# Kernel tuning notes

Measured on AMD Instinct MI355X. Metric: run time of the kernel, lower is better.

## Reference

```python
import jax, jax.numpy as jnp
import numpy as np

N_NODES = 50000
N_EDGES = 800000
IN_FEATS = 64
H_FEATS = 128


def _uniform(key, shape, stdv):
    return jax.random.uniform(key, shape, jnp.float32, -stdv, stdv)


def setup_inputs() -> dict:
    key = jax.random.key(0)
    ks = jax.random.split(key, 16)
    inp = {}
    inp["features"] = jax.random.normal(ks[0], (N_NODES, IN_FEATS), jnp.float32)
    inp["mask"] = (jax.random.uniform(ks[1], (N_NODES, IN_FEATS)) > 0.3).astype(jnp.float32)
    inp["norm_g"] = jax.random.uniform(ks[2], (N_NODES, 1), jnp.float32, 0.05, 1.0)
    inp["norm_f"] = jax.random.uniform(ks[3], (N_NODES, 1), jnp.float32, 0.05, 1.0)
    inp["src_g"] = jax.random.randint(ks[4], (N_EDGES,), 0, N_NODES, jnp.int32)
    inp["dst_g"] = jax.random.randint(ks[5], (N_EDGES,), 0, N_NODES, jnp.int32)
    inp["src_f"] = jax.random.randint(ks[6], (N_EDGES,), 0, N_NODES, jnp.int32)
    inp["dst_f"] = jax.random.randint(ks[7], (N_EDGES,), 0, N_NODES, jnp.int32)
    # learned params, init per reset_parameters (uniform +/- 1/sqrt(out_feats))
    s1 = 1.0 / np.sqrt(H_FEATS)
    inp["W1"] = _uniform(ks[8], (IN_FEATS, H_FEATS), s1)
    inp["b1"] = _uniform(ks[9], (H_FEATS,), s1)
    s2 = 1.0 / np.sqrt(IN_FEATS)
    inp["wh"] = _uniform(ks[10], (H_FEATS, IN_FEATS), s2)
    inp["bh"] = _uniform(ks[11], (IN_FEATS,), s2)
    inp["ws"] = _uniform(ks[12], (IN_FEATS, IN_FEATS), s2)
    inp["bs"] = _uniform(ks[13], (IN_FEATS,), s2)
    return inp


def _aggregate(h, src, dst):
    # DGL update_all(copy_src, sum): gather source node feats per edge, sum at dst
    return jax.ops.segment_sum(h[src], dst, num_segments=N_NODES)


def reference(features, mask, norm_g, norm_f, src_g, dst_g, src_f, dst_f,
              W1, b1, wh, bh, ws, bs):
    x = features * mask                     # [N, in]
    # GCL (masked_gcn)
    h = (x @ W1) * norm_g                   # [N, h]
    h = _aggregate(h, src_g, dst_g) * norm_g + b1
    h = jax.nn.relu(h)
    # GCL_skip (output_gcn): h branch on g, skip branch s on f
    hb = (h @ wh) * norm_g                  # [N, in]
    sb = (x @ ws) * norm_f                  # [N, in]
    hb = _aggregate(hb, src_g, dst_g) * norm_g + bh
    sb = _aggregate(sb, src_f, dst_f) * norm_f + bs
    return jax.nn.sigmoid(hb + sb)
```

## Files before the change

### kernel.cpp

```cpp
#include <hip/hip_runtime.h>
#include <hip/hip_fp16.h>

#define N_NODES 50000
#define N_EDGES 800000
#define IN_F 64
#define H_F 128
#define NBUK 98
#define CAPB 12288
#define EPB 2048
#define NBLK 391

typedef unsigned short u16;
typedef unsigned int u32;

static __device__ __forceinline__ float4 ld4(const float* p) {
    return *reinterpret_cast<const float4*>(p);
}
static __device__ __forceinline__ void st4(float* p, float4 v) {
    *reinterpret_cast<float4*>(p) = v;
}
static __device__ __forceinline__ void st_h4(__half* p, float4 v) {
    union { __half h[4]; uint2 u; } pk;
    pk.h[0] = __float2half_rn(v.x);
    pk.h[1] = __float2half_rn(v.y);
    pk.h[2] = __float2half_rn(v.z);
    pk.h[3] = __float2half_rn(v.w);
    *reinterpret_cast<uint2*>(p) = pk.u;
}
static __device__ __forceinline__ void add_h8(float4& a, float4& b, uint4 r) {
    __half2* p = reinterpret_cast<__half2*>(&r);
    float2 f0 = __half22float2(p[0]);
    float2 f1 = __half22float2(p[1]);
    float2 f2 = __half22float2(p[2]);
    float2 f3 = __half22float2(p[3]);
    a.x += f0.x; a.y += f0.y; a.z += f1.x; a.w += f1.y;
    b.x += f2.x; b.y += f2.y; b.z += f3.x; b.w += f3.y;
}
static __device__ __forceinline__ void unpack8(uint4 u, float* w) {
    const __half2* hp = reinterpret_cast<const __half2*>(&u);
    float2 f0 = __half22float2(hp[0]);
    float2 f1 = __half22float2(hp[1]);
    float2 f2 = __half22float2(hp[2]);
    float2 f3 = __half22float2(hp[3]);
    w[0] = f0.x; w[1] = f0.y; w[2] = f1.x; w[3] = f1.y;
    w[4] = f2.x; w[5] = f2.y; w[6] = f3.x; w[7] = f3.y;
}

__global__ __launch_bounds__(256) void part_k(
    const int* __restrict__ src_g, const int* __restrict__ dst_g, u32* __restrict__ rec_g,
    const int* __restrict__ src_f, const int* __restrict__ dst_f, u32* __restrict__ rec_f,
    int* __restrict__ bukcur,
    const float* __restrict__ f, const float* __restrict__ m,
    const float* __restrict__ ng, __half* __restrict__ y)
{
    __shared__ int c[NBUK];
    __shared__ int base[NBUK];
    const int tid = threadIdx.x;
    const int graph = blockIdx.x >= NBLK;
    const int blk = blockIdx.x - graph * NBLK;
    const int* src = graph ? src_f : src_g;
    const int* dst = graph ? dst_f : dst_g;
    u32* rec = graph ? rec_f : rec_g;
    int* cur = bukcur + graph * NBUK;

    if (tid < NBUK) c[tid] = 0;
    __syncthreads();
    const int e0 = blk * EPB;
    const int e1 = min(e0 + EPB, N_EDGES);

    u32 r_[8];
    bool v_[8];
#pragma unroll
    for (int j = 0; j < 8; ++j) {
        int e = e0 + tid + j * 256;
        v_[j] = (e < e1);
        int d = 0, s = 0;
        if (v_[j]) { d = dst[e]; s = src[e]; }
        r_[j] = ((u32)s << 16) | (u32)d;
        if (v_[j]) atomicAdd(&c[d >> 9], 1);
    }
    __syncthreads();
    if (tid < NBUK) base[tid] = atomicAdd(&cur[tid], c[tid]);
    __syncthreads();
    if (tid < NBUK) c[tid] = 0;
    __syncthreads();
#pragma unroll
    for (int j = 0; j < 8; ++j) {
        if (v_[j]) {
            u32 r = r_[j];
            int b = (int)((r & 0xFFFFu) >> 9);
            int p = base[b] + atomicAdd(&c[b], 1);
            if (p < CAPB) rec[b * CAPB + p] = r;
        }
    }
    for (int i = blockIdx.x * 256 + tid; i < N_NODES * (IN_F / 4);
         i += gridDim.x * 256) {
        int n = i >> 4;
        float s = ng[n];
        float4 a = ld4(f + 4 * i);
        float4 b = ld4(m + 4 * i);
        float4 r;
        r.x = a.x * b.x * s; r.y = a.y * b.y * s;
        r.z = a.z * b.z * s; r.w = a.w * b.w * s;
        st_h4(y + 4 * i, r);
    }
}

__global__ __launch_bounds__(512) void p3_build_k(
    const u32* __restrict__ rec_g, int* __restrict__ rps_g, int* __restrict__ rpe_g,
    u16* __restrict__ adj_g,
    const u32* __restrict__ rec_f, int* __restrict__ rps_f, int* __restrict__ rpe_f,
    u16* __restrict__ adj_f,
    const int* __restrict__ bukcur)
{
    __shared__ int hist[512];
    __shared__ int tmp[512];
    const int tid = threadIdx.x;
    const int graph = blockIdx.x >= NBUK;
    const int b = blockIdx.x - graph * NBUK;
    const u32* rec = graph ? rec_f : rec_g;
    int* rps = graph ? rps_f : rps_g;
    int* rpe = graph ? rpe_f : rpe_g;
    u16* adj = graph ? adj_f : adj_g;
    const int e_base = b * CAPB;
    const int e_cnt  = min(bukcur[graph * NBUK + b], CAPB);

    hist[tid] = 0;
    __syncthreads();
    for (int i = tid; i < e_cnt; i += 512)
        atomicAdd(&hist[rec[e_base + i] & 511], 1);
    __syncthreads();
    const int v = hist[tid];
    tmp[tid] = v;
    __syncthreads();
    for (int o = 1; o < 512; o <<= 1) {
        int t = (tid >= o) ? tmp[tid - o] : 0;
        __syncthreads();
        tmp[tid] += t;
        __syncthreads();
    }
    const int incl = tmp[tid];
    const int excl = incl - v;
    const int n = (b << 9) + tid;
    if (n < N_NODES) {
        rps[n] = e_base + excl;
        rpe[n] = e_base + incl;
    }
    hist[tid] = excl;
    __syncthreads();
    for (int i = tid; i < e_cnt; i += 512) {
        u32 r = rec[e_base + i];
        int p = atomicAdd(&hist[r & 511], 1);
        adj[e_base + p] = (u16)(r >> 16);
    }
}

__global__ __launch_bounds__(256) void fused_mlp_k(
    const __half* __restrict__ y,
    const int* __restrict__ rps, const int* __restrict__ rpe,
    const u16* __restrict__ adj,
    const float* __restrict__ W1, const float* __restrict__ b1,
    const float* __restrict__ wh, const float* __restrict__ ng,
    __half* __restrict__ hb0, int M)
{
    __shared__ __align__(16) __half WlH[8192];
    __shared__ __align__(16) float  Al[64 * 65];
    __shared__ __align__(16) __half Ah[64 * 130];

    const int tid = threadIdx.x;
    const int n0  = blockIdx.x << 6;

    for (int i = tid; i < 2048; i += 256) st_h4(&WlH[4 * i], ld4(W1 + 4 * i));

    {
        const int node = tid >> 2, q = tid & 3;
        const int gn = n0 + node;
        float4 A0 = make_float4(0.f, 0.f, 0.f, 0.f);
        float4 A1 = make_float4(0.f, 0.f, 0.f, 0.f);
        float4 A2 = make_float4(0.f, 0.f, 0.f, 0.f);
        float4 A3 = make_float4(0.f, 0.f, 0.f, 0.f);
        if (gn < M) {
            int e = rps[gn];
            const int e1 = rpe[gn];
            const __half* base = y + (q << 4);
            for (; e + 2 <= e1; e += 2) {
                const __half* ra = base + ((int)adj[e] << 6);
                const __half* rb = base + ((int)adj[e + 1] << 6);
                uint4 a0 = *reinterpret_cast<const uint4*>(ra);
                uint4 a1 = *reinterpret_cast<const uint4*>(ra + 8);
                uint4 b0 = *reinterpret_cast<const uint4*>(rb);
                uint4 b1v = *reinterpret_cast<const uint4*>(rb + 8);
                add_h8(A0, A1, a0); add_h8(A2, A3, a1);
                add_h8(A0, A1, b0); add_h8(A2, A3, b1v);
            }
            for (; e < e1; ++e) {
                const __half* ra = base + ((int)adj[e] << 6);
                uint4 a0 = *reinterpret_cast<const uint4*>(ra);
                uint4 a1 = *reinterpret_cast<const uint4*>(ra + 8);
                add_h8(A0, A1, a0); add_h8(A2, A3, a1);
            }
        }
        float* p = &Al[node * 65 + (q << 4)];
        p[0]  = A0.x; p[1]  = A0.y; p[2]  = A0.z; p[3]  = A0.w;
        p[4]  = A1.x; p[5]  = A1.y; p[6]  = A1.z; p[7]  = A1.w;
        p[8]  = A2.x; p[9]  = A2.y; p[10] = A2.z; p[11] = A2.w;
        p[12] = A3.x; p[13] = A3.y; p[14] = A3.z; p[15] = A3.w;
    }
    __syncthreads();

    const int tr = tid & 15;
    const int tc = tid >> 4;
    float ngv[4];
#pragma unroll
    for (int i = 0; i < 4; ++i) {
        int gn = n0 + 4 * tr + i;
        ngv[i] = (gn < M) ? ng[gn] : 0.f;
    }

    float acc1[4][8];
#pragma unroll
    for (int i = 0; i < 4; ++i)
#pragma unroll
        for (int j = 0; j < 8; ++j) acc1[i][j] = 0.f;
#pragma unroll 4
    for (int k = 0; k < 64; ++k) {
        float a0 = Al[(4 * tr + 0) * 65 + k];
        float a1 = Al[(4 * tr + 1) * 65 + k];
        float a2 = Al[(4 * tr + 2) * 65 + k];
        float a3 = Al[(4 * tr + 3) * 65 + k];
        uint4 wu = *reinterpret_cast<const uint4*>(&WlH[k * 128 + tc * 8]);
        float wv[8];
        unpack8(wu, wv);
#pragma unroll
        for (int j = 0; j < 8; ++j) {
            acc1[0][j] += a0 * wv[j];
            acc1[1][j] += a1 * wv[j];
            acc1[2][j] += a2 * wv[j];
            acc1[3][j] += a3 * wv[j];
        }
    }
    __syncthreads();

    {
        float4 bA = ld4(b1 + tc * 8);
        float4 bB = ld4(b1 + tc * 8 + 4);
#pragma unroll
        for (int i = 0; i < 4; ++i) {
            union { __half h[8]; u32 w[4]; } pk;
            float s = ngv[i];
            pk.h[0] = __float2half_rn(fmaxf(fmaf(acc1[i][0], s, bA.x), 0.f));
            pk.h[1] = __float2half_rn(fmaxf(fmaf(acc1[i][1], s, bA.y), 0.f));
            pk.h[2] = __float2half_rn(fmaxf(fmaf(acc1[i][2], s, bA.z), 0.f));
            pk.h[3] = __float2half_rn(fmaxf(fmaf(acc1[i][3], s, bA.w), 0.f));
            pk.h[4] = __float2half_rn(fmaxf(fmaf(acc1[i][4], s, bB.x), 0.f));
            pk.h[5] = __float2half_rn(fmaxf(fmaf(acc1[i][5], s, bB.y), 0.f));
            pk.h[6] = __float2half_rn(fmaxf(fmaf(acc1[i][6], s, bB.z), 0.f));
            pk.h[7] = __float2half_rn(fmaxf(fmaf(acc1[i][7], s, bB.w), 0.f));
            u32* dst = reinterpret_cast<u32*>(&Ah[(4 * tr + i) * 130 + tc * 8]);
            dst[0] = pk.w[0]; dst[1] = pk.w[1]; dst[2] = pk.w[2]; dst[3] = pk.w[3];
        }
        for (int i = tid; i < 2048; i += 256) st_h4(&WlH[4 * i], ld4(wh + 4 * i));
    }
    __syncthreads();

    float acc2[4][4];
#pragma unroll
    for (int i = 0; i < 4; ++i)
#pragma unroll
        for (int j = 0; j < 4; ++j) acc2[i][j] = 0.f;
#pragma unroll 4
    for (int k2 = 0; k2 < 64; ++k2) {
        u32 a0u = *reinterpret_cast<const u32*>(&Ah[(4 * tr + 0) * 130 + 2 * k2]);
        u32 a1u = *reinterpret_cast<const u32*>(&Ah[(4 * tr + 1) * 130 + 2 * k2]);
        u32 a2u = *reinterpret_cast<const u32*>(&Ah[(4 * tr + 2) * 130 + 2 * k2]);
        u32 a3u = *reinterpret_cast<const u32*>(&Ah[(4 * tr + 3) * 130 + 2 * k2]);
        float2 a0 = __half22float2(*reinterpret_cast<const __half2*>(&a0u));
        float2 a1 = __half22float2(*reinterpret_cast<const __half2*>(&a1u));
        float2 a2 = __half22float2(*reinterpret_cast<const __half2*>(&a2u));
        float2 a3 = __half22float2(*reinterpret_cast<const __half2*>(&a3u));
        uint2 wau = *reinterpret_cast<const uint2*>(&WlH[(2 * k2) * 64 + tc * 4]);
        uint2 wbu = *reinterpret_cast<const uint2*>(&WlH[(2 * k2 + 1) * 64 + tc * 4]);
        const __half2* wap = reinterpret_cast<const __half2*>(&wau);
        const __half2* wbp = reinterpret_cast<const __half2*>(&wbu);
        float2 wa0 = __half22float2(wap[0]), wa1 = __half22float2(wap[1]);
        float2 wb0 = __half22float2(wbp[0]), wb1 = __half22float2(wbp[1]);
        float wva[4] = { wa0.x, wa0.y, wa1.x, wa1.y };
        float wvb[4] = { wb0.x, wb0.y, wb1.x, wb1.y };
#pragma unroll
        for (int j = 0; j < 4; ++j) {
            acc2[0][j] += a0.x * wva[j] + a0.y * wvb[j];
            acc2[1][j] += a1.x * wva[j] + a1.y * wvb[j];
            acc2[2][j] += a2.x * wva[j] + a2.y * wvb[j];
            acc2[3][j] += a3.x * wva[j] + a3.y * wvb[j];
        }
    }
#pragma unroll
    for (int i = 0; i < 4; ++i) {
        int gn = n0 + 4 * tr + i;
        if (gn >= M) continue;
        float s = ngv[i];
        float4 o;
        o.x = acc2[i][0] * s; o.y = acc2[i][1] * s;
        o.z = acc2[i][2] * s; o.w = acc2[i][3] * s;
        st_h4(hb0 + (gn << 6) + tc * 4, o);
    }
}

static __device__ __forceinline__ void csr_row_sum_h8(
        const __half* __restrict__ tbl, const u16* __restrict__ adj,
        int e, int e1, int off, float4& A, float4& B) {
    for (; e + 4 <= e1; e += 4) {
        int s0 = adj[e], s1 = adj[e + 1], s2 = adj[e + 2], s3 = adj[e + 3];
        uint4 r0 = *reinterpret_cast<const uint4*>(tbl + (s0 << 6) + off);
        uint4 r1 = *reinterpret_cast<const uint4*>(tbl + (s1 << 6) + off);
        uint4 r2 = *reinterpret_cast<const uint4*>(tbl + (s2 << 6) + off);
        uint4 r3 = *reinterpret_cast<const uint4*>(tbl + (s3 << 6) + off);
        add_h8(A, B, r0); add_h8(A, B, r1); add_h8(A, B, r2); add_h8(A, B, r3);
    }
    for (; e < e1; ++e) {
        uint4 r = *reinterpret_cast<const uint4*>(tbl + (adj[e] << 6) + off);
        add_h8(A, B, r);
    }
}

template<int K, int N, int SMODE, int EPI, int OUT16>
__global__ __launch_bounds__(256) void gemm_k(
    const float* __restrict__ A, const float* __restrict__ A2,
    const float* __restrict__ W, const float* __restrict__ rs,
    const float* __restrict__ bias, void* __restrict__ outv, int M)
{
    constexpr int CPT = N / 16;
    constexpr int AS  = K + 1;
    constexpr int KQ  = K / 4;
    __shared__ __align__(16) float Wl[K * N];
    __shared__ __align__(16) float Al[64 * AS];

    const int tid = threadIdx.x;
    const int n0  = blockIdx.x << 6;

    for (int i = tid; i < K * N / 4; i += 256) st4(&Wl[4 * i], ld4(W + 4 * i));
    for (int i4 = tid; i4 < 64 * KQ; i4 += 256) {
        int n  = i4 / KQ;
        int k4 = (i4 & (KQ - 1)) << 2;
        int gn = n0 + n;
        float4 v = make_float4(0.f, 0.f, 0.f, 0.f);
        if (gn < M) {
            v = ld4(A + gn * K + k4);
            if (SMODE == 1) {
                float4 m4 = ld4(A2 + gn * K + k4);
                v.x *= m4.x; v.y *= m4.y; v.z *= m4.z; v.w *= m4.w;
            }
        }
        float* p = &Al[n * AS + k4];
        p[0] = v.x; p[1] = v.y; p[2] = v.z; p[3] = v.w;
    }
    __syncthreads();

    const int tr = tid & 15;
    const int tc = tid >> 4;

    float acc[4][CPT];
#pragma unroll
    for (int i = 0; i < 4; ++i)
#pragma unroll
        for (int j = 0; j < CPT; ++j) acc[i][j] = 0.f;

#pragma unroll 4
    for (int k = 0; k < K; ++k) {
        float a0 = Al[(4 * tr + 0) * AS + k];
        float a1 = Al[(4 * tr + 1) * AS + k];
        float a2 = Al[(4 * tr + 2) * AS + k];
        float a3 = Al[(4 * tr + 3) * AS + k];
#pragma unroll
        for (int jq = 0; jq < CPT / 4; ++jq) {
            float4 w = ld4(&Wl[k * N + tc * CPT + 4 * jq]);
            acc[0][4 * jq + 0] += a0 * w.x; acc[0][4 * jq + 1] += a0 * w.y;
            acc[0][4 * jq + 2] += a0 * w.z; acc[0][4 * jq + 3] += a0 * w.w;
            acc[1][4 * jq + 0] += a1 * w.x; acc[1][4 * jq + 1] += a1 * w.y;
            acc[1][4 * jq + 2] += a1 * w.z; acc[1][4 * jq + 3] += a1 * w.w;
            acc[2][4 * jq + 0] += a2 * w.x; acc[2][4 * jq + 1] += a2 * w.y;
            acc[2][4 * jq + 2] += a2 * w.z; acc[2][4 * jq + 3] += a2 * w.w;
            acc[3][4 * jq + 0] += a3 * w.x; acc[3][4 * jq + 1] += a3 * w.y;
            acc[3][4 * jq + 2] += a3 * w.z; acc[3][4 * jq + 3] += a3 * w.w;
        }
    }

#pragma unroll
    for (int i = 0; i < 4; ++i) {
        int gn = n0 + 4 * tr + i;
        if (gn >= M) continue;
        float s = rs[gn];
#pragma unroll
        for (int jq = 0; jq < CPT / 4; ++jq) {
            float4 o;
            if (EPI == 1) {
                float4 b4 = ld4(bias + tc * CPT + 4 * jq);
                o.x = fmaxf(fmaf(acc[i][4 * jq + 0], s, b4.x), 0.f);
                o.y = fmaxf(fmaf(acc[i][4 * jq + 1], s, b4.y), 0.f);
                o.z = fmaxf(fmaf(acc[i][4 * jq + 2], s, b4.z), 0.f);
                o.w = fmaxf(fmaf(acc[i][4 * jq + 3], s, b4.w), 0.f);
            } else {
                o.x = acc[i][4 * jq + 0] * s; o.y = acc[i][4 * jq + 1] * s;
                o.z = acc[i][4 * jq + 2] * s; o.w = acc[i][4 * jq + 3] * s;
            }
            if (OUT16) {
                st_h4((__half*)outv + gn * N + tc * CPT + 4 * jq, o);
            } else {
                st4((float*)outv + gn * N + tc * CPT + 4 * jq, o);
            }
        }
    }
}

__global__ __launch_bounds__(256) void final2_k(
    const __half* __restrict__ hb, const __half* __restrict__ sb,
    const int* __restrict__ rps_g, const int* __restrict__ rpe_g,
    const u16* __restrict__ adj_g,
    const int* __restrict__ rps_f, const int* __restrict__ rpe_f,
    const u16* __restrict__ adj_f,
    const float* __restrict__ ng, const float* __restrict__ nf,
    const float* __restrict__ bh, const float* __restrict__ bs,
    float* __restrict__ out)
{
    const int tid = threadIdx.x;
    const int fl = tid & 7;
    const int n  = blockIdx.x * 32 + (tid >> 3);
    if (n >= N_NODES) return;
    const int off = fl << 3;
    float4 Ag = make_float4(0.f, 0.f, 0.f, 0.f);
    float4 Bg = make_float4(0.f, 0.f, 0.f, 0.f);
    float4 Af = make_float4(0.f, 0.f, 0.f, 0.f);
    float4 Bf = make_float4(0.f, 0.f, 0.f, 0.f);
    csr_row_sum_h8(hb, adj_g, rps_g[n], rpe_g[n], off, Ag, Bg);
    csr_row_sum_h8(sb, adj_f, rps_f[n], rpe_f[n], off, Af, Bf);
    const float g = ng[n], f = nf[n];
    float4 b0 = ld4(bh + off), b1 = ld4(bh + off + 4);
    float4 s0 = ld4(bs + off), s1 = ld4(bs + off + 4);
    float4 o0, o1;
    float t;
    t = Ag.x * g + b0.x + Af.x * f + s0.x; o0.x = 1.f / (1.f + expf(-t));
    t = Ag.y * g + b0.y + Af.y * f + s0.y; o0.y = 1.f / (1.f + expf(-t));
    t = Ag.z * g + b0.z + Af.z * f + s0.z; o0.z = 1.f / (1.f + expf(-t));
    t = Ag.w * g + b0.w + Af.w * f + s0.w; o0.w = 1.f / (1.f + expf(-t));
    t = Bg.x * g + b1.x + Bf.x * f + s1.x; o1.x = 1.f / (1.f + expf(-t));
    t = Bg.y * g + b1.y + Bf.y * f + s1.y; o1.y = 1.f / (1.f + expf(-t));
    t = Bg.z * g + b1.z + Bf.z * f + s1.z; o1.z = 1.f / (1.f + expf(-t));
    t = Bg.w * g + b1.w + Bf.w * f + s1.w; o1.w = 1.f / (1.f + expf(-t));
    st4(out + (n << 6) + off, o0);
    st4(out + (n << 6) + off + 4, o1);
}

extern "C" void kernel_launch(void* const* d_in, const int* in_sizes, int n_in,
                              void* d_out, int out_size, void* d_ws, size_t ws_size,
                              hipStream_t stream) {
    const float* features = (const float*)d_in[0];
    const float* mask     = (const float*)d_in[1];
    const float* norm_g   = (const float*)d_in[2];
    const float* norm_f   = (const float*)d_in[3];
    const int*   src_g    = (const int*)d_in[4];
    const int*   dst_g    = (const int*)d_in[5];
    const int*   src_f    = (const int*)d_in[6];
    const int*   dst_f    = (const int*)d_in[7];
    const float* W1  = (const float*)d_in[8];
    const float* b1  = (const float*)d_in[9];
    const float* wh  = (const float*)d_in[10];
    const float* bh  = (const float*)d_in[11];
    const float* wsw = (const float*)d_in[12];
    const float* bs  = (const float*)d_in[13];
    float* out = (float*)d_out;
    float* ws  = (float*)d_ws;

    __half* y   = (__half*)ws;
    __half* hb0 = (__half*)(ws + 1600000);
    __half* sb0 = (__half*)(ws + 3200000);
    int* creg   = (int*)(ws + 6400000);
    u32* rec_g  = (u32*)creg;
    u32* rec_f  = rec_g + NBUK * CAPB;
    int* bukcur = (int*)(rec_f + NBUK * CAPB);
    int* pers   = (int*)(ws + 12800000);
    int* rps_g  = pers;
    int* rpe_g  = pers + 50000;
    int* rps_f  = pers + 100000;
    int* rpe_f  = pers + 150000;
    u16* adj_g  = (u16*)(pers + 200000);
    u16* adj_f  = adj_g + NBUK * CAPB;

    const int gblocks = (N_NODES + 63) / 64;
    const int nblk32  = (N_NODES + 31) / 32;

    hipMemsetAsync(bukcur, 0, 2 * NBUK * sizeof(int), stream);
    part_k<<<2 * NBLK, 256, 0, stream>>>(src_g, dst_g, rec_g,
                                         src_f, dst_f, rec_f, bukcur,
                                         features, mask, norm_g, y);
    p3_build_k<<<2 * NBUK, 512, 0, stream>>>(rec_g, rps_g, rpe_g, adj_g,
                                             rec_f, rps_f, rpe_f, adj_f, bukcur);

    fused_mlp_k<<<gblocks, 256, 0, stream>>>(y, rps_g, rpe_g, adj_g,
                                             W1, b1, wh, norm_g, hb0, N_NODES);

    gemm_k<64, 64, 1, 2, 1><<<gblocks, 256, 0, stream>>>(features, mask, wsw, norm_f,
                                                         nullptr, (void*)sb0, N_NODES);

    final2_k<<<nblk32, 256, 0, stream>>>(hb0, sb0, rps_g, rpe_g, adj_g,
                                         rps_f, rpe_f, adj_f,
                                         norm_g, norm_f, bh, bs, out);
}
```

Measured before the change: 238.5 us.

## Split fused aggregation+MLP into separate gather kernel and MLP kernel

Moves the first-layer neighbor aggregation out of the fused MLP kernel into its own kernel, which uses 8 threads per node with 16-byte loads and 32 nodes per block. The result goes to an fp16 intermediate buffer that the MLP kernel then reads coalesced. The first GEMM now reads fp16 pairs from shared memory, and the shared-memory row strides are padded. This aims at better latency hiding and occupancy for the irregular gather, which was limited by the GEMM's shared-memory use and 4 threads per node. The cost is an extra kernel launch and a round trip of the 50000x64 fp16 intermediate through global memory.

```diff
diff --git a/kernel.cpp b/kernel.cpp
--- a/kernel.cpp
+++ b/kernel.cpp
@@ -9,6 +9,8 @@
 #define CAPB 12288
 #define EPB 2048
 #define NBLK 391
+#define SA 66
+#define SH 134
 
 typedef unsigned short u16;
 typedef unsigned int u32;
@@ -155,56 +157,59 @@
     }
 }
 
-__global__ __launch_bounds__(256) void fused_mlp_k(
-    const __half* __restrict__ y,
-    const int* __restrict__ rps, const int* __restrict__ rpe,
-    const u16* __restrict__ adj,
+static __device__ __forceinline__ void csr_row_sum_h8(
+        const __half* __restrict__ tbl, const u16* __restrict__ adj,
+        int e, int e1, int off, float4& A, float4& B) {
+    for (; e + 4 <= e1; e += 4) {
+        int s0 = adj[e], s1 = adj[e + 1], s2 = adj[e + 2], s3 = adj[e + 3];
+        uint4 r0 = *reinterpret_cast<const uint4*>(tbl + (s0 << 6) + off);
+        uint4 r1 = *reinterpret_cast<const uint4*>(tbl + (s1 << 6) + off);
+        uint4 r2 = *reinterpret_cast<const uint4*>(tbl + (s2 << 6) + off);
+        uint4 r3 = *reinterpret_cast<const uint4*>(tbl + (s3 << 6) + off);
+        add_h8(A, B, r0); add_h8(A, B, r1); add_h8(A, B, r2); add_h8(A, B, r3);
+    }
+    for (; e < e1; ++e) {
+        uint4 r = *reinterpret_cast<const uint4*>(tbl + (adj[e] << 6) + off);
+        add_h8(A, B, r);
+    }
+}
+
+__global__ __launch_bounds__(256) void agg64h_k(const __half* __restrict__ tbl,
+        const int* __restrict__ rps, const int* __restrict__ rpe,
+        const u16* __restrict__ adj, __half* __restrict__ out) {
+    const int tid = threadIdx.x;
+    const int fl = tid & 7;
+    const int n  = blockIdx.x * 32 + (tid >> 3);
+    if (n >= N_NODES) return;
+    const int off = fl << 3;
+    float4 A = make_float4(0.f, 0.f, 0.f, 0.f);
+    float4 B = make_float4(0.f, 0.f, 0.f, 0.f);
+    csr_row_sum_h8(tbl, adj, rps[n], rpe[n], off, A, B);
+    st_h4(out + (n << 6) + off, A);
+    st_h4(out + (n << 6) + off + 4, B);
+}
+
+__global__ __launch_bounds__(256) void mlp_k(
+    const __half* __restrict__ z,
     const float* __restrict__ W1, const float* __restrict__ b1,
     const float* __restrict__ wh, const float* __restrict__ ng,
     __half* __restrict__ hb0, int M)
 {
     __shared__ __align__(16) __half WlH[8192];
-    __shared__ __align__(16) float  Al[64 * 65];
-    __shared__ __align__(16) __half Ah[64 * 130];
+    __shared__ __align__(16) __half Al[64 * SA];
+    __shared__ __align__(16) __half Ah[64 * SH];
 
     const int tid = threadIdx.x;
     const int n0  = blockIdx.x << 6;
 
     for (int i = tid; i < 2048; i += 256) st_h4(&WlH[4 * i], ld4(W1 + 4 * i));
-
-    {
-        const int node = tid >> 2, q = tid & 3;
-        const int gn = n0 + node;
-        float4 A0 = make_float4(0.f, 0.f, 0.f, 0.f);
-        float4 A1 = make_float4(0.f, 0.f, 0.f, 0.f);
-        float4 A2 = make_float4(0.f, 0.f, 0.f, 0.f);
-        float4 A3 = make_float4(0.f, 0.f, 0.f, 0.f);
-        if (gn < M) {
-            int e = rps[gn];
-            const int e1 = rpe[gn];
-            const __half* base = y + (q << 4);
-            for (; e + 2 <= e1; e += 2) {
-                const __half* ra = base + ((int)adj[e] << 6);
-                const __half* rb = base + ((int)adj[e + 1] << 6);
-                uint4 a0 = *reinterpret_cast<const uint4*>(ra);
-                uint4 a1 = *reinterpret_cast<const uint4*>(ra + 8);
-                uint4 b0 = *reinterpret_cast<const uint4*>(rb);
-                uint4 b1v = *reinterpret_cast<const uint4*>(rb + 8);
-                add_h8(A0, A1, a0); add_h8(A2, A3, a1);
-                add_h8(A0, A1, b0); add_h8(A2, A3, b1v);
-            }
-            for (; e < e1; ++e) {
-                const __half* ra = base + ((int)adj[e] << 6);
-                uint4 a0 = *reinterpret_cast<const uint4*>(ra);
-                uint4 a1 = *reinterpret_cast<const uint4*>(ra + 8);
-                add_h8(A0, A1, a0); add_h8(A2, A3, a1);
-            }
-        }
-        float* p = &Al[node * 65 + (q << 4)];
-        p[0]  = A0.x; p[1]  = A0.y; p[2]  = A0.z; p[3]  = A0.w;
-        p[4]  = A1.x; p[5]  = A1.y; p[6]  = A1.z; p[7]  = A1.w;
-        p[8]  = A2.x; p[9]  = A2.y; p[10] = A2.z; p[11] = A2.w;
-        p[12] = A3.x; p[13] = A3.y; p[14] = A3.z; p[15] = A3.w;
+    for (int i = tid; i < 512; i += 256) {
+        int node = i >> 3, q = i & 7;
+        int gn = n0 + node;
+        uint4 v = make_uint4(0u, 0u, 0u, 0u);
+        if (gn < M) v = *reinterpret_cast<const uint4*>(z + (gn << 6) + (q << 3));
+        u32* d = reinterpret_cast<u32*>(&Al[node * SA + (q << 3)]);
+        d[0] = v.x; d[1] = v.y; d[2] = v.z; d[3] = v.w;
     }
     __syncthreads();
 
@@ -223,20 +228,26 @@
 #pragma unroll
         for (int j = 0; j < 8; ++j) acc1[i][j] = 0.f;
 #pragma unroll 4
-    for (int k = 0; k < 64; ++k) {
-        float a0 = Al[(4 * tr + 0) * 65 + k];
-        float a1 = Al[(4 * tr + 1) * 65 + k];
-        float a2 = Al[(4 * tr + 2) * 65 + k];
-        float a3 = Al[(4 * tr + 3) * 65 + k];
-        uint4 wu = *reinterpret_cast<const uint4*>(&WlH[k * 128 + tc * 8]);
-        float wv[8];
-        unpack8(wu, wv);
+    for (int k2 = 0; k2 < 32; ++k2) {
+        u32 a0u = *reinterpret_cast<const u32*>(&Al[(4 * tr + 0) * SA + 2 * k2]);
+        u32 a1u = *reinterpret_cast<const u32*>(&Al[(4 * tr + 1) * SA + 2 * k2]);
+        u32 a2u = *reinterpret_cast<const u32*>(&Al[(4 * tr + 2) * SA + 2 * k2]);
+        u32 a3u = *reinterpret_cast<const u32*>(&Al[(4 * tr + 3) * SA + 2 * k2]);
+        float2 a0 = __half22float2(*reinterpret_cast<const __half2*>(&a0u));
+        float2 a1 = __half22float2(*reinterpret_cast<const __half2*>(&a1u));
+        float2 a2 = __half22float2(*reinterpret_cast<const __half2*>(&a2u));
+        float2 a3 = __half22float2(*reinterpret_cast<const __half2*>(&a3u));
+        uint4 wua = *reinterpret_cast<const uint4*>(&WlH[(2 * k2) * 128 + tc * 8]);
+        uint4 wub = *reinterpret_cast<const uint4*>(&WlH[(2 * k2 + 1) * 128 + tc * 8]);
+        float wa[8], wb[8];
+        unpack8(wua, wa);
+        unpack8(wub, wb);
 #pragma unroll
         for (int j = 0; j < 8; ++j) {
-            acc1[0][j] += a0 * wv[j];
-            acc1[1][j] += a1 * wv[j];
-            acc1[2][j] += a2 * wv[j];
-            acc1[3][j] += a3 * wv[j];
+            acc1[0][j] += a0.x * wa[j] + a0.y * wb[j];
+            acc1[1][j] += a1.x * wa[j] + a1.y * wb[j];
+            acc1[2][j] += a2.x * wa[j] + a2.y * wb[j];
+            acc1[3][j] += a3.x * wa[j] + a3.y * wb[j];
         }
     }
     __syncthreads();
@@ -256,7 +267,7 @@
             pk.h[5] = __float2half_rn(fmaxf(fmaf(acc1[i][5], s, bB.y), 0.f));
             pk.h[6] = __float2half_rn(fmaxf(fmaf(acc1[i][6], s, bB.z), 0.f));
             pk.h[7] = __float2half_rn(fmaxf(fmaf(acc1[i][7], s, bB.w), 0.f));
-            u32* dst = reinterpret_cast<u32*>(&Ah[(4 * tr + i) * 130 + tc * 8]);
+            u32* dst = reinterpret_cast<u32*>(&Ah[(4 * tr + i) * SH + tc * 8]);
             dst[0] = pk.w[0]; dst[1] = pk.w[1]; dst[2] = pk.w[2]; dst[3] = pk.w[3];
         }
         for (int i = tid; i < 2048; i += 256) st_h4(&WlH[4 * i], ld4(wh + 4 * i));
@@ -270,10 +281,10 @@
         for (int j = 0; j < 4; ++j) acc2[i][j] = 0.f;
 #pragma unroll 4
     for (int k2 = 0; k2 < 64; ++k2) {
-        u32 a0u = *reinterpret_cast<const u32*>(&Ah[(4 * tr + 0) * 130 + 2 * k2]);
-        u32 a1u = *reinterpret_cast<const u32*>(&Ah[(4 * tr + 1) * 130 + 2 * k2]);
-        u32 a2u = *reinterpret_cast<const u32*>(&Ah[(4 * tr + 2) * 130 + 2 * k2]);
-        u32 a3u = *reinterpret_cast<const u32*>(&Ah[(4 * tr + 3) * 130 + 2 * k2]);
+        u32 a0u = *reinterpret_cast<const u32*>(&Ah[(4 * tr + 0) * SH + 2 * k2]);
+        u32 a1u = *reinterpret_cast<const u32*>(&Ah[(4 * tr + 1) * SH + 2 * k2]);
+        u32 a2u = *reinterpret_cast<const u32*>(&Ah[(4 * tr + 2) * SH + 2 * k2]);
+        u32 a3u = *reinterpret_cast<const u32*>(&Ah[(4 * tr + 3) * SH + 2 * k2]);
         float2 a0 = __half22float2(*reinterpret_cast<const __half2*>(&a0u));
         float2 a1 = __half22float2(*reinterpret_cast<const __half2*>(&a1u));
         float2 a2 = __half22float2(*reinterpret_cast<const __half2*>(&a2u));
@@ -303,23 +314,6 @@
         o.x = acc2[i][0] * s; o.y = acc2[i][1] * s;
         o.z = acc2[i][2] * s; o.w = acc2[i][3] * s;
         st_h4(hb0 + (gn << 6) + tc * 4, o);
-    }
-}
-
-static __device__ __forceinline__ void csr_row_sum_h8(
-        const __half* __restrict__ tbl, const u16* __restrict__ adj,
-        int e, int e1, int off, float4& A, float4& B) {
-    for (; e + 4 <= e1; e += 4) {
-        int s0 = adj[e], s1 = adj[e + 1], s2 = adj[e + 2], s3 = adj[e + 3];
-        uint4 r0 = *reinterpret_cast<const uint4*>(tbl + (s0 << 6) + off);
-        uint4 r1 = *reinterpret_cast<const uint4*>(tbl + (s1 << 6) + off);
-        uint4 r2 = *reinterpret_cast<const uint4*>(tbl + (s2 << 6) + off);
-        uint4 r3 = *reinterpret_cast<const uint4*>(tbl + (s3 << 6) + off);
-        add_h8(A, B, r0); add_h8(A, B, r1); add_h8(A, B, r2); add_h8(A, B, r3);
-    }
-    for (; e < e1; ++e) {
-        uint4 r = *reinterpret_cast<const uint4*>(tbl + (adj[e] << 6) + off);
-        add_h8(A, B, r);
     }
 }
 
@@ -473,6 +467,7 @@
     __half* y   = (__half*)ws;
     __half* hb0 = (__half*)(ws + 1600000);
     __half* sb0 = (__half*)(ws + 3200000);
+    __half* z   = (__half*)(ws + 4800000);
     int* creg   = (int*)(ws + 6400000);
     u32* rec_g  = (u32*)creg;
     u32* rec_f  = rec_g + NBUK * CAPB;
@@ -495,8 +490,9 @@
     p3_build_k<<<2 * NBUK, 512, 0, stream>>>(rec_g, rps_g, rpe_g, adj_g,
                                              rec_f, rps_f, rpe_f, adj_f, bukcur);
 
-    fused_mlp_k<<<gblocks, 256, 0, stream>>>(y, rps_g, rpe_g, adj_g,
-                                             W1, b1, wh, norm_g, hb0, N_NODES);
+    agg64h_k<<<nblk32, 256, 0, stream>>>(y, rps_g, rpe_g, adj_g, z);
+
+    mlp_k<<<gblocks, 256, 0, stream>>>(z, W1, b1, wh, norm_g, hb0, N_NODES);
 
     gemm_k<64, 64, 1, 2, 1><<<gblocks, 256, 0, stream>>>(features, mask, wsw, norm_f,
                                                          nullptr, (void*)sb0, N_NODES);
```

Measured after the change: 240.4 us. No clear change (+0.8%).
